# Kernel tuning notes

Hardware: AMD Instinct MI355X
Metric: run time of the kernel (lower is better)

Reference implementation:

```python
import jax, jax.numpy as jnp
import numpy as np

B, N, G, K, C = 16, 8192, 128, 32, 384
EPS = 1e-5


def _fps(xyz, n):
    # furthest point sampling starting at index 0 (matches pointnet2 CUDA op)
    b = xyz.shape[0]
    dists = jnp.sum((xyz - xyz[:, :1]) ** 2, -1)  # [B,N] dist^2 to first pt

    def step(d, _):
        idx = jnp.argmax(d, axis=-1)                       # [B]
        p = jnp.take_along_axis(xyz, idx[:, None, None], 1)  # [B,1,3]
        d = jnp.minimum(d, jnp.sum((xyz - p) ** 2, -1))
        return d, idx.astype(jnp.int32)

    _, idxs = jax.lax.scan(step, dists, None, length=n - 1)
    idx = jnp.concatenate([jnp.zeros((1, b), jnp.int32), idxs], 0).T  # [B,n]
    return jnp.take_along_axis(xyz, idx[..., None], axis=1)


def _morton_order(center):
    # greedy nearest-neighbour tour over group centers (simplied_morton_sorting)
    b, g, _ = center.shape
    d = jnp.sum((center[:, :, None] - center[:, None]) ** 2, -1)  # [B,G,G]
    d = jnp.where(jnp.eye(g, dtype=bool), jnp.inf, d)

    def step(carry, _):
        cur, visited = carry
        row = jnp.take_along_axis(d, cur[:, None, None], 1)[:, 0]  # [B,G]
        row = jnp.where(visited, jnp.inf, row)
        nxt = jnp.argmin(row, -1).astype(jnp.int32)
        visited = visited | jax.nn.one_hot(nxt, g, dtype=bool)
        return (nxt, visited), nxt

    cur0 = jnp.zeros((b,), jnp.int32)
    init = (cur0, jax.nn.one_hot(cur0, g, dtype=bool))
    _, nxts = jax.lax.scan(step, init, None, length=g - 1)
    return jnp.concatenate([jnp.zeros((1, b), jnp.int32), nxts], 0).T  # [B,G]


def _bn(x, g_, b_, m_, v_):
    return (x - m_) * (g_ * jax.lax.rsqrt(v_ + EPS)) + b_


def _pos_embed(center):
    npf = 128  # 384 // 3 // 2 * 2
    i = jnp.arange(npf, dtype=jnp.float32)
    dim_t = 10000.0 ** (2.0 * jnp.floor(i / 2) / npf)
    x = center * (2.0 * np.pi)
    pd = x[..., None] / dim_t                                # [B,G,3,128]
    emb = jnp.stack([jnp.sin(pd[..., 0::2]), jnp.cos(pd[..., 1::2])], -1)
    return emb.reshape(*center.shape[:-1], -1)               # [B,G,384]


def _forward(xyz, w1, b1, g1, bt1, m1, v1, w2, b2, w3, b3, g3, bt3, m3, v3, w4, b4):
    center = _fps(xyz, G)                                    # [B,G,3]
    # squared-distance KNN (argsort order identical to euclidean cdist)
    d2 = (jnp.sum(center ** 2, -1)[:, :, None]
          + jnp.sum(xyz ** 2, -1)[:, None]
          - 2.0 * jnp.einsum('bgd,bnd->bgn', center, xyz))   # [B,G,N]
    _, idx = jax.lax.top_k(-d2, K)                           # [B,G,K]
    neigh = jnp.take_along_axis(xyz, idx.reshape(B, G * K)[..., None], 1)
    neigh = neigh.reshape(B, G, K, 3) - center[:, :, None]
    order = _morton_order(center)                            # [B,G]
    neigh = jnp.take_along_axis(neigh, order[:, :, None, None], 1)
    center = jnp.take_along_axis(center, order[:, :, None], 1)
    # Encoder_small (1x1 convs == per-point linears, eval-mode BN)
    pg = neigh.reshape(B * G, K, 3)
    f = jax.nn.relu(_bn(pg @ w1.T + b1, g1, bt1, m1, v1)) @ w2.T + b2  # [BG,K,256]
    fg = jnp.max(f, 1, keepdims=True)
    h = jnp.concatenate([jnp.broadcast_to(fg, f.shape), f], -1)        # [BG,K,512]
    h = jax.nn.relu(_bn(h @ w3.T + b3, g3, bt3, m3, v3)) @ w4.T + b4   # [BG,K,384]
    tokens = jnp.max(h, 1).reshape(B, G, C)
    return tokens + _pos_embed(center)


def setup_inputs() -> dict:
    key = jax.random.key(0)
    ks = jax.random.split(key, 8)
    s = 0.05
    return {
        'xyz': jax.random.normal(ks[0], (B, N, 3), jnp.float32),
        'w1': jax.random.normal(ks[1], (128, 3), jnp.float32) * s,
        'b1': jax.random.normal(ks[2], (128,), jnp.float32) * s,
        'g1': jnp.ones((128,), jnp.float32),
        'bt1': jnp.zeros((128,), jnp.float32),
        'm1': jnp.zeros((128,), jnp.float32),
        'v1': jnp.ones((128,), jnp.float32),
        'w2': jax.random.normal(ks[3], (256, 128), jnp.float32) * s,
        'b2': jax.random.normal(ks[4], (256,), jnp.float32) * s,
        'w3': jax.random.normal(ks[5], (512, 512), jnp.float32) * s,
        'b3': jnp.zeros((512,), jnp.float32),
        'g3': jnp.ones((512,), jnp.float32),
        'bt3': jnp.zeros((512,), jnp.float32),
        'm3': jnp.zeros((512,), jnp.float32),
        'v3': jnp.ones((512,), jnp.float32),
        'w4': jax.random.normal(ks[6], (384, 512), jnp.float32) * s,
        'b4': jax.random.normal(ks[7], (384,), jnp.float32) * s,
    }


def reference(xyz, w1, b1, g1, bt1, m1, v1, w2, b2, w3, b3, g3, bt3, m3, v3, w4, b4):
    return _forward(xyz, w1, b1, g1, bt1, m1, v1, w2, b2, w3, b3, g3, bt3, m3, v3, w4, b4)
```

## Files before the change

kernel.cpp:

```cpp
#include <hip/hip_runtime.h>
#include <hip/hip_bf16.h>

#define B_ 16
#define N_ 8192
#define G_ 128
#define K_ 32
#define C_ 384
#define EPSV 1e-5f

typedef __attribute__((ext_vector_type(8))) short bf16x8;
typedef __attribute__((ext_vector_type(8))) unsigned short u16x8;
typedef __attribute__((ext_vector_type(4))) float f32x4;
typedef __attribute__((ext_vector_type(2))) float f32x2;

__device__ __forceinline__ unsigned short f2b(float f){
  unsigned int u = __float_as_uint(f);
  u += 0x7fffu + ((u >> 16) & 1u);
  return (unsigned short)(u >> 16);
}
__device__ __forceinline__ float b2f(unsigned short s){
  return __uint_as_float(((unsigned int)s) << 16);
}
__device__ __forceinline__ float sq3(float dx, float dy, float dz){
  return __fadd_rn(__fadd_rn(__fmul_rn(dx,dx), __fmul_rn(dy,dy)), __fmul_rn(dz,dz));
}
__device__ __forceinline__ f32x2 pkmax(f32x2 a, f32x2 b){
  return f32x2{fmaxf(a.x,b.x), fmaxf(a.y,b.y)};
}
__device__ __forceinline__ unsigned fenc(float f){
  unsigned u = __float_as_uint(f);
  return ((int)u >= 0) ? (u | 0x80000000u) : ~u;
}

#define DPP_MAXU_STAGE(r, CTRL) { \
  unsigned _o = (unsigned)__builtin_amdgcn_update_dpp((int)(r), (int)(r), (CTRL), 0xf, 0xf, false); \
  (r) = ((r) > _o) ? (r) : _o; }
#define DPP_MAXU_ALL(r) \
  DPP_MAXU_STAGE(r, 0x111) DPP_MAXU_STAGE(r, 0x112) DPP_MAXU_STAGE(r, 0x114) \
  DPP_MAXU_STAGE(r, 0x118) DPP_MAXU_STAGE(r, 0x142) DPP_MAXU_STAGE(r, 0x143)
#define DPP_MINU_STAGE(r, CTRL) { \
  unsigned _o = (unsigned)__builtin_amdgcn_update_dpp((int)(r), (int)(r), (CTRL), 0xf, 0xf, false); \
  (r) = ((r) < _o) ? (r) : _o; }
#define DPP_MINU_ALL(r) \
  DPP_MINU_STAGE(r, 0x111) DPP_MINU_STAGE(r, 0x112) DPP_MINU_STAGE(r, 0x114) \
  DPP_MINU_STAGE(r, 0x118) DPP_MINU_STAGE(r, 0x142) DPP_MINU_STAGE(r, 0x143)

__global__ __launch_bounds__(256) void prep_kernel(
    const float* __restrict__ w2, const float* __restrict__ w3,
    const float* __restrict__ w4, unsigned short* __restrict__ w2b,
    unsigned short* __restrict__ w3b, unsigned short* __restrict__ w4b){
  int i = blockIdx.x*256 + threadIdx.x;
  if (i < 32768){ w2b[i] = f2b(w2[i]); return; }
  i -= 32768;
  if (i < 262144){ w3b[i] = f2b(w3[i]); return; }
  i -= 262144;
  if (i < 196608){ w4b[i] = f2b(w4[i]); }
}

__attribute__((amdgpu_flat_work_group_size(256,256), amdgpu_waves_per_eu(1,1)))
__global__ void fps_morton_kernel(const float* __restrict__ xyz,
                                  float* __restrict__ centers_ord){
  const int b = blockIdx.x, t = threadIdx.x, w = t >> 6;
  const int lane = t & 63;
  const float* xb = xyz + (size_t)b*N_*3;
  __shared__ __align__(16) float sval[2][4];
  __shared__ __align__(16) int   sidx[2][4];
  __shared__ float clx[G_], cly[G_], clz[G_];
  const int base = t*32;
  f32x2 X[16], Y[16], Z[16], D[16];
  const float p0x = xb[0], p0y = xb[1], p0z = xb[2];
  {
#pragma clang fp contract(off)
    float s[96];
    const float4* src = (const float4*)(xb + (size_t)base*3);
    #pragma unroll
    for (int q = 0; q < 24; q++) ((float4*)s)[q] = src[q];
    #pragma unroll
    for (int p = 0; p < 16; p++){
      X[p] = f32x2{s[6*p+0], s[6*p+3]};
      Y[p] = f32x2{s[6*p+1], s[6*p+4]};
      Z[p] = f32x2{s[6*p+2], s[6*p+5]};
      const f32x2 dx = X[p] - p0x, dy = Y[p] - p0y, dz = Z[p] - p0z;
      D[p] = (dx*dx + dy*dy) + dz*dz;
    }
  }
  if (t == 0){ clx[0] = p0x; cly[0] = p0y; clz[0] = p0z; }
  int buf = 0;
  for (int g = 1; g < G_; g++){
    const f32x2 mm = pkmax(pkmax(pkmax(pkmax(D[0],D[1]),pkmax(D[2],D[3])),
                                 pkmax(pkmax(D[4],D[5]),pkmax(D[6],D[7]))),
                           pkmax(pkmax(pkmax(D[8],D[9]),pkmax(D[10],D[11])),
                                 pkmax(pkmax(D[12],D[13]),pkmax(D[14],D[15]))));
    const float v = fmaxf(mm.x, mm.y);
    int jl = 0;
    #pragma unroll
    for (int p = 15; p >= 0; p--){
      if (D[p].y == v) jl = 2*p+1;
      if (D[p].x == v) jl = 2*p;
    }
    const unsigned uv = __float_as_uint(v);
    unsigned r = uv;
    DPP_MAXU_ALL(r)
    const unsigned wmax = (unsigned)__builtin_amdgcn_readlane((int)r, 63);
    const unsigned long long tie = __ballot(uv == wmax);
    const int wl = __ffsll(tie) - 1;
    if (lane == wl){ sval[buf][w] = __uint_as_float(wmax); sidx[buf][w] = base + jl; }
    __syncthreads();
    const float4 vv = *(const float4*)&sval[buf][0];
    const int4   ii = *(const int4*)&sidx[buf][0];
    float bv = vv.x; int bb = ii.x;
    if (vv.y > bv){ bv = vv.y; bb = ii.y; }
    if (vv.z > bv){ bv = vv.z; bb = ii.z; }
    if (vv.w > bv){ bv = vv.w; bb = ii.w; }
    {
#pragma clang fp contract(off)
      const int ubb = __builtin_amdgcn_readfirstlane(bb);
      const float cx = xb[ubb*3], cy = xb[ubb*3+1], cz = xb[ubb*3+2];
      if (t == 0){ clx[g] = cx; cly[g] = cy; clz[g] = cz; }
      #pragma unroll
      for (int p = 0; p < 16; p++){
        const f32x2 dx = X[p] - cx, dy = Y[p] - cy, dz = Z[p] - cz;
        const f32x2 dn = (dx*dx + dy*dy) + dz*dz;
        D[p] = f32x2{fminf(D[p].x, dn.x), fminf(D[p].y, dn.y)};
      }
    }
    buf ^= 1;
  }
  __syncthreads();
  if (t < 64){
    float mcx[2], mcy[2], mcz[2]; bool mvis[2];
    #pragma unroll
    for (int j = 0; j < 2; j++){
      const int idx = lane + j*64;
      mcx[j] = clx[idx]; mcy[j] = cly[idx]; mcz[j] = clz[idx];
      mvis[j] = (idx == 0);
    }
    float curx = clx[0], cury = cly[0], curz = clz[0];
    if (lane == 0){
      centers_ord[(size_t)b*G_*3 + 0] = curx;
      centers_ord[(size_t)b*G_*3 + 1] = cury;
      centers_ord[(size_t)b*G_*3 + 2] = curz;
    }
    for (int step = 1; step < G_; step++){
      const float d0r = sq3(__fsub_rn(mcx[0],curx), __fsub_rn(mcy[0],cury), __fsub_rn(mcz[0],curz));
      const float d1r = sq3(__fsub_rn(mcx[1],curx), __fsub_rn(mcy[1],cury), __fsub_rn(mcz[1],curz));
      const float d0 = mvis[0] ? __builtin_inff() : d0r;
      const float d1 = mvis[1] ? __builtin_inff() : d1r;
      float mv = d0; int mi = lane;
      if (d1 < mv){ mv = d1; mi = lane + 64; }
      const int wj = mi >> 6;
      const float sx = wj ? mcx[1] : mcx[0];
      const float sy = wj ? mcy[1] : mcy[0];
      const float sz = wj ? mcz[1] : mcz[0];
      const unsigned key = __float_as_uint(mv);
      unsigned r = key;
      DPP_MINU_ALL(r)
      const unsigned wmin = (unsigned)__builtin_amdgcn_readlane((int)r, 63);
      const unsigned long long tie = __ballot(key == wmin);
      int wl;
      if (__popcll(tie) == 1){
        wl = __ffsll(tie) - 1;
      } else {
        float tv = mv; int ti = mi;
        #pragma unroll
        for (int mk = 1; mk < 64; mk <<= 1){
          const float ov = __shfl_xor(tv, mk);
          const int   oi = __shfl_xor(ti, mk);
          if (ov < tv || (ov == tv && oi < ti)){ tv = ov; ti = oi; }
        }
        wl = ti & 63;
      }
      const int mbi = __builtin_amdgcn_readlane(mi, wl);
      curx = __uint_as_float((unsigned)__builtin_amdgcn_readlane((int)__float_as_uint(sx), wl));
      cury = __uint_as_float((unsigned)__builtin_amdgcn_readlane((int)__float_as_uint(sy), wl));
      curz = __uint_as_float((unsigned)__builtin_amdgcn_readlane((int)__float_as_uint(sz), wl));
      if (lane == wl){
        if ((mbi >> 6) == 0) mvis[0] = true; else mvis[1] = true;
      }
      if (lane == 0){
        centers_ord[((size_t)b*G_ + step)*3 + 0] = curx;
        centers_ord[((size_t)b*G_ + step)*3 + 1] = cury;
        centers_ord[((size_t)b*G_ + step)*3 + 2] = curz;
      }
    }
  }
}

__global__ __launch_bounds__(256, 2) void knn_kernel(const float* __restrict__ xyz,
                                                     const float* __restrict__ centers_ord,
                                                     float* __restrict__ neigh){
  const int gp = blockIdx.x, b = blockIdx.y, t = threadIdx.x;
  const int lane = t & 63, w = t >> 6;
  __shared__ __align__(16) float sv[2][4];
  __shared__ __align__(16) int   si[2][4];
  __shared__ int list[K_];
  const float* xb = xyz + (size_t)b*N_*3;
  const float* cp = centers_ord + ((size_t)b*G_ + gp)*3;
  const float cxv = cp[0], cyv = cp[1], czv = cp[2];
  const float cc = sq3(cxv, cyv, czv);
  const int base = t*32;
  float dd[32];
  float v = __builtin_inff(); int jl = 0;
  {
    float s[96];
    const float4* src = (const float4*)(xb + (size_t)base*3);
    #pragma unroll
    for (int q = 0; q < 24; q++) ((float4*)s)[q] = src[q];
    #pragma unroll
    for (int j = 0; j < 32; j++){
      const float x = s[3*j], y = s[3*j+1], z = s[3*j+2];
      const float xx = sq3(x, y, z);
      const float dot = __fadd_rn(__fadd_rn(__fmul_rn(cxv,x), __fmul_rn(cyv,y)), __fmul_rn(czv,z));
      dd[j] = __fsub_rn(__fadd_rn(cc, xx), __fmul_rn(2.f, dot));
      if (dd[j] < v){ v = dd[j]; jl = j; }
    }
  }
  int buf = 0;
  for (int it = 0; it < K_; it++){
    const unsigned key = fenc(v);
    unsigned r = key;
    DPP_MINU_ALL(r)
    const unsigned wmin = (unsigned)__builtin_amdgcn_readlane((int)r, 63);
    const unsigned long long tie = __ballot(key == wmin);
    const int wl = __ffsll(tie) - 1;
    if (lane == wl){ sv[buf][w] = v; si[buf][w] = base + jl; }
    __syncthreads();
    const float4 vv = *(const float4*)&sv[buf][0];
    const int4   ii = *(const int4*)&si[buf][0];
    float bv = vv.x; int bb = ii.x;
    if (vv.y < bv){ bv = vv.y; bb = ii.y; }
    if (vv.z < bv){ bv = vv.z; bb = ii.z; }
    if (vv.w < bv){ bv = vv.w; bb = ii.w; }
    if (t == 0) list[it] = bb;
    if ((bb >> 5) == t){
      const int jw = bb & 31;
      #pragma unroll
      for (int j = 0; j < 32; j++) if (j == jw) dd[j] = __builtin_inff();
      v = __builtin_inff(); jl = 0;
      #pragma unroll
      for (int j = 0; j < 32; j++) if (dd[j] < v){ v = dd[j]; jl = j; }
    }
    buf ^= 1;
  }
  __syncthreads();
  if (t < K_*3){
    const int k = t / 3, d = t % 3;
    const int n = list[k];
    neigh[(((size_t)b*G_ + gp)*K_ + k)*3 + d] = __fsub_rn(xb[n*3+d], cp[d]);
  }
}

__device__ __forceinline__ int swzF(int row, int col){
  int byteo = row*512 + col*2;
  byteo ^= (row & 7) << 4;
  return byteo >> 1;
}
__device__ __forceinline__ int swzA(int row, int col){
  int byteo = row*1024 + col*2;
  byteo ^= (row & 7) << 4;
  return byteo >> 1;
}

__global__ __launch_bounds__(256, 2) void enc_kernel(
    const float* __restrict__ neigh, const float* __restrict__ centers_ord,
    const float* __restrict__ w1, const float* __restrict__ b1,
    const float* __restrict__ g1, const float* __restrict__ bt1,
    const float* __restrict__ m1, const float* __restrict__ v1,
    const unsigned short* __restrict__ w2b, const float* __restrict__ b2,
    const unsigned short* __restrict__ w3b, const float* __restrict__ b3,
    const float* __restrict__ g3, const float* __restrict__ bt3,
    const float* __restrict__ m3, const float* __restrict__ v3,
    const unsigned short* __restrict__ w4b, const float* __restrict__ b4,
    float* __restrict__ out)
{
  const int gp = blockIdx.x, b = blockIdx.y, t = threadIdx.x;
  const int lane = t & 63, w = t >> 6, lr = lane & 15, lg = lane >> 4;
  __shared__ __align__(16) unsigned short Fl[32*256];
  __shared__ __align__(16) unsigned short A3[32*512];
  __shared__ __align__(16) unsigned short fgb[256];
  __shared__ float pg[96];
  __shared__ float ctr[3];
  float* tok = (float*)Fl;

  const int gid = b*G_ + gp;
  if (t < 96) pg[t] = neigh[(size_t)gid*96 + t];
  if (t < 3)  ctr[t] = centers_ord[(size_t)gid*3 + t];
  __syncthreads();

  bf16x8 a1f[2][4];
  #pragma unroll
  for (int kt = 0; kt < 4; kt++){
    #pragma unroll
    for (int j = 0; j < 8; j++){
      const int c = kt*32 + lg*8 + j;
      const float wx = w1[c*3], wy = w1[c*3+1], wz = w1[c*3+2];
      const float sc = g1[c] * rsqrtf(v1[c] + EPSV);
      const float mm = m1[c], bb = bt1[c], bc = b1[c];
      #pragma unroll
      for (int mt = 0; mt < 2; mt++){
        const int p = mt*16 + lr;
        float v = pg[p*3]*wx + pg[p*3+1]*wy + pg[p*3+2]*wz + bc;
        v = (v - mm)*sc + bb;
        v = fmaxf(v, 0.f);
        a1f[mt][kt][j] = (short)f2b(v);
      }
    }
  }

  const int n0w = w*64;
  {
    bf16x8 Bk[16];
    #pragma unroll
    for (int i = 0; i < 16; i++){
      const int nt = i >> 2, kt = i & 3;
      Bk[i] = *(const bf16x8*)(w2b + (size_t)(n0w + nt*16 + lr)*128 + kt*32 + lg*8);
    }
    f32x4 accB[2][4];
    #pragma unroll
    for (int mt = 0; mt < 2; mt++)
      #pragma unroll
      for (int nt = 0; nt < 4; nt++){
        f32x4 z = {0.f,0.f,0.f,0.f};
        accB[mt][nt] = z;
      }
    #pragma unroll
    for (int nt = 0; nt < 4; nt++)
      #pragma unroll
      for (int kt = 0; kt < 4; kt++){
        accB[0][nt] = __builtin_amdgcn_mfma_f32_16x16x32_bf16(a1f[0][kt], Bk[nt*4+kt], accB[0][nt], 0,0,0);
        accB[1][nt] = __builtin_amdgcn_mfma_f32_16x16x32_bf16(a1f[1][kt], Bk[nt*4+kt], accB[1][nt], 0,0,0);
      }
    #pragma unroll
    for (int nt = 0; nt < 4; nt++){
      const int col = n0w + nt*16 + lr;
      const float bc = b2[col];
      #pragma unroll
      for (int mt = 0; mt < 2; mt++)
        #pragma unroll
        for (int r = 0; r < 4; r++){
          const int row = mt*16 + lg*4 + r;
          Fl[swzF(row,col)] = f2b(accB[mt][nt][r] + bc);
        }
    }
  }
  __syncthreads();

  {
    float mx = -__builtin_inff();
    #pragma unroll 4
    for (int row = 0; row < 32; row++) mx = fmaxf(mx, b2f(Fl[swzF(row, t)]));
    fgb[t] = f2b(mx);
  }
  __syncthreads();

  {
    bf16x8 afg[8], afl0[8], afl1[8];
    #pragma unroll
    for (int k8 = 0; k8 < 8; k8++){
      afg[k8]  = *(const bf16x8*)&fgb[k8*32 + lg*8];
      afl0[k8] = *(const bf16x8*)&Fl[swzF(lr,      k8*32 + lg*8)];
      afl1[k8] = *(const bf16x8*)&Fl[swzF(16 + lr, k8*32 + lg*8)];
    }
    #pragma unroll
    for (int nt = 0; nt < 8; nt++){
      const int col = w*128 + nt*16 + lr;
      const unsigned short* wr = w3b + (size_t)col*512;
      bf16x8 Bk[16];
      #pragma unroll
      for (int kt = 0; kt < 16; kt++) Bk[kt] = *(const bf16x8*)(wr + kt*32 + lg*8);
      f32x4 a0 = {0.f,0.f,0.f,0.f}, a1v = {0.f,0.f,0.f,0.f};
      #pragma unroll
      for (int k8 = 0; k8 < 8; k8++){
        a0  = __builtin_amdgcn_mfma_f32_16x16x32_bf16(afg[k8], Bk[k8], a0, 0,0,0);
        a1v = __builtin_amdgcn_mfma_f32_16x16x32_bf16(afg[k8], Bk[k8], a1v, 0,0,0);
      }
      #pragma unroll
      for (int k8 = 0; k8 < 8; k8++){
        a0  = __builtin_amdgcn_mfma_f32_16x16x32_bf16(afl0[k8], Bk[8+k8], a0, 0,0,0);
        a1v = __builtin_amdgcn_mfma_f32_16x16x32_bf16(afl1[k8], Bk[8+k8], a1v, 0,0,0);
      }
      const float bc = b3[col];
      const float sc = g3[col]*rsqrtf(v3[col] + EPSV);
      const float mm = m3[col], bb = bt3[col];
      #pragma unroll
      for (int mt = 0; mt < 2; mt++)
        #pragma unroll
        for (int r = 0; r < 4; r++){
          const int row = mt*16 + lg*4 + r;
          float v = (mt ? a1v[r] : a0[r]) + bc;
          v = (v - mm)*sc + bb;
          v = fmaxf(v, 0.f);
          A3[swzA(row,col)] = f2b(v);
        }
    }
  }
  __syncthreads();

  {
    bf16x8 aa0[16], aa1[16];
    #pragma unroll
    for (int kt = 0; kt < 16; kt++){
      aa0[kt] = *(const bf16x8*)&A3[swzA(lr,      kt*32 + lg*8)];
      aa1[kt] = *(const bf16x8*)&A3[swzA(16 + lr, kt*32 + lg*8)];
    }
    #pragma unroll
    for (int nt = 0; nt < 6; nt++){
      const int col = w*96 + nt*16 + lr;
      const unsigned short* wr = w4b + (size_t)col*512;
      bf16x8 Bk[16];
      #pragma unroll
      for (int kt = 0; kt < 16; kt++) Bk[kt] = *(const bf16x8*)(wr + kt*32 + lg*8);
      f32x4 a0 = {0.f,0.f,0.f,0.f}, a1v = {0.f,0.f,0.f,0.f};
      #pragma unroll
      for (int kt = 0; kt < 16; kt++){
        a0  = __builtin_amdgcn_mfma_f32_16x16x32_bf16(aa0[kt], Bk[kt], a0, 0,0,0);
        a1v = __builtin_amdgcn_mfma_f32_16x16x32_bf16(aa1[kt], Bk[kt], a1v, 0,0,0);
      }
      float mx = fmaxf(fmaxf(fmaxf(a0[0],a0[1]), fmaxf(a0[2],a0[3])),
                       fmaxf(fmaxf(a1v[0],a1v[1]), fmaxf(a1v[2],a1v[3])));
      mx = fmaxf(mx, __shfl_xor(mx, 16));
      mx = fmaxf(mx, __shfl_xor(mx, 32));
      if (lg == 0) tok[col] = mx + b4[col];
    }
  }
  __syncthreads();

  for (int c = t; c < C_; c += 256){
    const int d = c >> 7, r = c & 127, m2 = r >> 1;
    const float e = (float)(2*m2) * (1.f/128.f);
    const float dimt = powf(10000.f, e);
    const float x2 = __fmul_rn(ctr[d], 6.28318530717958647692f);
    const float ang = __fdiv_rn(x2, dimt);
    out[(size_t)gid*C_ + c] = tok[c] + ((r & 1) ? cosf(ang) : sinf(ang));
  }
}

extern "C" void kernel_launch(void* const* d_in, const int* in_sizes, int n_in,
                              void* d_out, int out_size, void* d_ws, size_t ws_size,
                              hipStream_t stream){
  (void)in_sizes; (void)n_in; (void)out_size; (void)ws_size;
  const float* xyz = (const float*)d_in[0];
  const float* w1  = (const float*)d_in[1];
  const float* b1  = (const float*)d_in[2];
  const float* g1  = (const float*)d_in[3];
  const float* bt1 = (const float*)d_in[4];
  const float* m1  = (const float*)d_in[5];
  const float* v1  = (const float*)d_in[6];
  const float* w2  = (const float*)d_in[7];
  const float* b2  = (const float*)d_in[8];
  const float* w3  = (const float*)d_in[9];
  const float* b3  = (const float*)d_in[10];
  const float* g3  = (const float*)d_in[11];
  const float* bt3 = (const float*)d_in[12];
  const float* m3  = (const float*)d_in[13];
  const float* v3  = (const float*)d_in[14];
  const float* w4  = (const float*)d_in[15];
  const float* b4  = (const float*)d_in[16];

  char* ws = (char*)d_ws;
  float* centers_ord  = (float*)(ws + 24576);
  float* neigh        = (float*)(ws + 49152);
  unsigned short* w2b = (unsigned short*)(ws + 835584);
  unsigned short* w3b = (unsigned short*)(ws + 901120);
  unsigned short* w4b = (unsigned short*)(ws + 1425408);

  prep_kernel      <<<1920, 256, 0, stream>>>(w2, w3, w4, w2b, w3b, w4b);
  fps_morton_kernel<<<B_, 256, 0, stream>>>(xyz, centers_ord);
  knn_kernel       <<<dim3(G_, B_), 256, 0, stream>>>(xyz, centers_ord, neigh);
  enc_kernel       <<<dim3(G_, B_), 256, 0, stream>>>(neigh, centers_ord,
      w1, b1, g1, bt1, m1, v1, w2b, b2, w3b, b3, g3, bt3, m3, v3, w4b, b4,
      (float*)d_out);
}
```

Baseline: 595.1 us.

## Process two groups per encoder block to share weight loads across MFMAs

The encoder kernel now handles two point groups per block with 512 threads. Each weight fragment loaded from global memory feeds MFMAs for both groups, which halves weight traffic per group. The first layer's activations are staged through shared memory instead of registers, and the column split across eight waves is changed. Shared memory per block roughly doubles, which may limit occupancy.

Measured after the change: 511.2 us. -14.1%, faster.

```diff
diff --git a/kernel.cpp b/kernel.cpp
--- a/kernel.cpp
+++ b/kernel.cpp
@@ -250,6 +250,11 @@
   }
 }
 
+__device__ __forceinline__ int swzA1(int row, int col){
+  int byteo = row*256 + col*2;
+  byteo ^= (row & 7) << 4;
+  return byteo >> 1;
+}
 __device__ __forceinline__ int swzF(int row, int col){
   int byteo = row*512 + col*2;
   byteo ^= (row & 7) << 4;
@@ -261,7 +266,7 @@
   return byteo >> 1;
 }
 
-__global__ __launch_bounds__(256, 2) void enc_kernel(
+__global__ __launch_bounds__(512, 2) void enc_kernel(
     const float* __restrict__ neigh, const float* __restrict__ centers_ord,
     const float* __restrict__ w1, const float* __restrict__ b1,
     const float* __restrict__ g1, const float* __restrict__ bt1,
@@ -273,165 +278,201 @@
     const unsigned short* __restrict__ w4b, const float* __restrict__ b4,
     float* __restrict__ out)
 {
-  const int gp = blockIdx.x, b = blockIdx.y, t = threadIdx.x;
+  const int t = threadIdx.x;
   const int lane = t & 63, w = t >> 6, lr = lane & 15, lg = lane >> 4;
-  __shared__ __align__(16) unsigned short Fl[32*256];
-  __shared__ __align__(16) unsigned short A3[32*512];
-  __shared__ __align__(16) unsigned short fgb[256];
-  __shared__ float pg[96];
-  __shared__ float ctr[3];
-  float* tok = (float*)Fl;
-
-  const int gid = b*G_ + gp;
-  if (t < 96) pg[t] = neigh[(size_t)gid*96 + t];
-  if (t < 3)  ctr[t] = centers_ord[(size_t)gid*3 + t];
-  __syncthreads();
-
-  bf16x8 a1f[2][4];
-  #pragma unroll
-  for (int kt = 0; kt < 4; kt++){
-    #pragma unroll
-    for (int j = 0; j < 8; j++){
-      const int c = kt*32 + lg*8 + j;
+  const int gid0 = blockIdx.x*2;
+  __shared__ __align__(16) unsigned short A1s[2][32*128];
+  __shared__ __align__(16) unsigned short Fl[2][32*256];
+  __shared__ __align__(16) unsigned short A3s[2][32*512];
+  __shared__ __align__(16) unsigned short fgb[2][256];
+  float* tokp = (float*)&Fl[0][0];
+
+  {
+    const int g = t >> 8, rem = t & 255, p = rem >> 3, c0 = (rem & 7) * 16;
+    const float* pgp = neigh + (size_t)(gid0 + g)*96 + p*3;
+    const float px = pgp[0], py = pgp[1], pz = pgp[2];
+    unsigned short hv[16];
+    #pragma unroll
+    for (int cc = 0; cc < 16; cc++){
+      const int c = c0 + cc;
       const float wx = w1[c*3], wy = w1[c*3+1], wz = w1[c*3+2];
       const float sc = g1[c] * rsqrtf(v1[c] + EPSV);
-      const float mm = m1[c], bb = bt1[c], bc = b1[c];
-      #pragma unroll
-      for (int mt = 0; mt < 2; mt++){
-        const int p = mt*16 + lr;
-        float v = pg[p*3]*wx + pg[p*3+1]*wy + pg[p*3+2]*wz + bc;
-        v = (v - mm)*sc + bb;
-        v = fmaxf(v, 0.f);
-        a1f[mt][kt][j] = (short)f2b(v);
-      }
-    }
-  }
-
-  const int n0w = w*64;
-  {
-    bf16x8 Bk[16];
-    #pragma unroll
-    for (int i = 0; i < 16; i++){
-      const int nt = i >> 2, kt = i & 3;
-      Bk[i] = *(const bf16x8*)(w2b + (size_t)(n0w + nt*16 + lr)*128 + kt*32 + lg*8);
-    }
-    f32x4 accB[2][4];
-    #pragma unroll
-    for (int mt = 0; mt < 2; mt++)
-      #pragma unroll
-      for (int nt = 0; nt < 4; nt++){
-        f32x4 z = {0.f,0.f,0.f,0.f};
-        accB[mt][nt] = z;
-      }
-    #pragma unroll
-    for (int nt = 0; nt < 4; nt++)
-      #pragma unroll
-      for (int kt = 0; kt < 4; kt++){
-        accB[0][nt] = __builtin_amdgcn_mfma_f32_16x16x32_bf16(a1f[0][kt], Bk[nt*4+kt], accB[0][nt], 0,0,0);
-        accB[1][nt] = __builtin_amdgcn_mfma_f32_16x16x32_bf16(a1f[1][kt], Bk[nt*4+kt], accB[1][nt], 0,0,0);
-      }
-    #pragma unroll
-    for (int nt = 0; nt < 4; nt++){
-      const int col = n0w + nt*16 + lr;
+      float val = px*wx + py*wy + pz*wz + b1[c];
+      val = (val - m1[c])*sc + bt1[c];
+      hv[cc] = f2b(fmaxf(val, 0.f));
+    }
+    *(u16x8*)&A1s[g][swzA1(p, c0)]     = *(u16x8*)&hv[0];
+    *(u16x8*)&A1s[g][swzA1(p, c0 + 8)] = *(u16x8*)&hv[8];
+  }
+  __syncthreads();
+
+  {
+    const int col0 = w*32;
+    f32x4 acc[2][2][2];
+    #pragma unroll
+    for (int nt = 0; nt < 2; nt++)
+      #pragma unroll
+      for (int g = 0; g < 2; g++)
+        #pragma unroll
+        for (int m = 0; m < 2; m++){ f32x4 z = {0.f,0.f,0.f,0.f}; acc[nt][g][m] = z; }
+    #pragma unroll
+    for (int kt = 0; kt < 4; kt++){
+      bf16x8 bA[2][2];
+      #pragma unroll
+      for (int g = 0; g < 2; g++)
+        #pragma unroll
+        for (int m = 0; m < 2; m++)
+          bA[g][m] = *(const bf16x8*)&A1s[g][swzA1(m*16 + lr, kt*32 + lg*8)];
+      bf16x8 bB[2];
+      #pragma unroll
+      for (int nt = 0; nt < 2; nt++)
+        bB[nt] = *(const bf16x8*)(w2b + (size_t)(col0 + nt*16 + lr)*128 + kt*32 + lg*8);
+      #pragma unroll
+      for (int nt = 0; nt < 2; nt++)
+        #pragma unroll
+        for (int g = 0; g < 2; g++)
+          #pragma unroll
+          for (int m = 0; m < 2; m++)
+            acc[nt][g][m] = __builtin_amdgcn_mfma_f32_16x16x32_bf16(bA[g][m], bB[nt], acc[nt][g][m], 0,0,0);
+    }
+    #pragma unroll
+    for (int nt = 0; nt < 2; nt++){
+      const int col = col0 + nt*16 + lr;
       const float bc = b2[col];
       #pragma unroll
-      for (int mt = 0; mt < 2; mt++)
-        #pragma unroll
-        for (int r = 0; r < 4; r++){
-          const int row = mt*16 + lg*4 + r;
-          Fl[swzF(row,col)] = f2b(accB[mt][nt][r] + bc);
-        }
-    }
-  }
-  __syncthreads();
-
-  {
+      for (int g = 0; g < 2; g++)
+        #pragma unroll
+        for (int m = 0; m < 2; m++)
+          #pragma unroll
+          for (int r = 0; r < 4; r++)
+            Fl[g][swzF(m*16 + lg*4 + r, col)] = f2b(acc[nt][g][m][r] + bc);
+    }
+  }
+  __syncthreads();
+
+  {
+    const int g = t >> 8, col = t & 255;
     float mx = -__builtin_inff();
     #pragma unroll 4
-    for (int row = 0; row < 32; row++) mx = fmaxf(mx, b2f(Fl[swzF(row, t)]));
-    fgb[t] = f2b(mx);
-  }
-  __syncthreads();
-
-  {
-    bf16x8 afg[8], afl0[8], afl1[8];
-    #pragma unroll
-    for (int k8 = 0; k8 < 8; k8++){
-      afg[k8]  = *(const bf16x8*)&fgb[k8*32 + lg*8];
-      afl0[k8] = *(const bf16x8*)&Fl[swzF(lr,      k8*32 + lg*8)];
-      afl1[k8] = *(const bf16x8*)&Fl[swzF(16 + lr, k8*32 + lg*8)];
-    }
-    #pragma unroll
-    for (int nt = 0; nt < 8; nt++){
-      const int col = w*128 + nt*16 + lr;
-      const unsigned short* wr = w3b + (size_t)col*512;
-      bf16x8 Bk[16];
-      #pragma unroll
-      for (int kt = 0; kt < 16; kt++) Bk[kt] = *(const bf16x8*)(wr + kt*32 + lg*8);
-      f32x4 a0 = {0.f,0.f,0.f,0.f}, a1v = {0.f,0.f,0.f,0.f};
-      #pragma unroll
-      for (int k8 = 0; k8 < 8; k8++){
-        a0  = __builtin_amdgcn_mfma_f32_16x16x32_bf16(afg[k8], Bk[k8], a0, 0,0,0);
-        a1v = __builtin_amdgcn_mfma_f32_16x16x32_bf16(afg[k8], Bk[k8], a1v, 0,0,0);
+    for (int row = 0; row < 32; row++) mx = fmaxf(mx, b2f(Fl[g][swzF(row, col)]));
+    fgb[g][col] = f2b(mx);
+  }
+  __syncthreads();
+
+  {
+    const int col0 = w*64;
+    f32x4 acc[4][2][2];
+    #pragma unroll
+    for (int nt = 0; nt < 4; nt++)
+      #pragma unroll
+      for (int g = 0; g < 2; g++)
+        #pragma unroll
+        for (int m = 0; m < 2; m++){ f32x4 z = {0.f,0.f,0.f,0.f}; acc[nt][g][m] = z; }
+    #pragma unroll
+    for (int kt = 0; kt < 16; kt++){
+      bf16x8 bA[2][2];
+      if (kt < 8){
+        #pragma unroll
+        for (int g = 0; g < 2; g++){
+          const bf16x8 af = *(const bf16x8*)&fgb[g][kt*32 + lg*8];
+          bA[g][0] = af; bA[g][1] = af;
+        }
+      } else {
+        #pragma unroll
+        for (int g = 0; g < 2; g++)
+          #pragma unroll
+          for (int m = 0; m < 2; m++)
+            bA[g][m] = *(const bf16x8*)&Fl[g][swzF(m*16 + lr, (kt-8)*32 + lg*8)];
       }
-      #pragma unroll
-      for (int k8 = 0; k8 < 8; k8++){
-        a0  = __builtin_amdgcn_mfma_f32_16x16x32_bf16(afl0[k8], Bk[8+k8], a0, 0,0,0);
-        a1v = __builtin_amdgcn_mfma_f32_16x16x32_bf16(afl1[k8], Bk[8+k8], a1v, 0,0,0);
-      }
+      bf16x8 bB[4];
+      #pragma unroll
+      for (int nt = 0; nt < 4; nt++)
+        bB[nt] = *(const bf16x8*)(w3b + (size_t)(col0 + nt*16 + lr)*512 + kt*32 + lg*8);
+      #pragma unroll
+      for (int nt = 0; nt < 4; nt++)
+        #pragma unroll
+        for (int g = 0; g < 2; g++)
+          #pragma unroll
+          for (int m = 0; m < 2; m++)
+            acc[nt][g][m] = __builtin_amdgcn_mfma_f32_16x16x32_bf16(bA[g][m], bB[nt], acc[nt][g][m], 0,0,0);
+    }
+    #pragma unroll
+    for (int nt = 0; nt < 4; nt++){
+      const int col = col0 + nt*16 + lr;
       const float bc = b3[col];
       const float sc = g3[col]*rsqrtf(v3[col] + EPSV);
       const float mm = m3[col], bb = bt3[col];
       #pragma unroll
-      for (int mt = 0; mt < 2; mt++)
-        #pragma unroll
-        for (int r = 0; r < 4; r++){
-          const int row = mt*16 + lg*4 + r;
-          float v = (mt ? a1v[r] : a0[r]) + bc;
-          v = (v - mm)*sc + bb;
-          v = fmaxf(v, 0.f);
-          A3[swzA(row,col)] = f2b(v);
-        }
-    }
-  }
-  __syncthreads();
-
-  {
-    bf16x8 aa0[16], aa1[16];
+      for (int g = 0; g < 2; g++)
+        #pragma unroll
+        for (int m = 0; m < 2; m++)
+          #pragma unroll
+          for (int r = 0; r < 4; r++){
+            float val = acc[nt][g][m][r] + bc;
+            val = (val - mm)*sc + bb;
+            A3s[g][swzA(m*16 + lg*4 + r, col)] = f2b(fmaxf(val, 0.f));
+          }
+    }
+  }
+  __syncthreads();
+
+  {
+    const int col0 = w*48;
+    f32x4 acc[3][2][2];
+    #pragma unroll
+    for (int nt = 0; nt < 3; nt++)
+      #pragma unroll
+      for (int g = 0; g < 2; g++)
+        #pragma unroll
+        for (int m = 0; m < 2; m++){ f32x4 z = {0.f,0.f,0.f,0.f}; acc[nt][g][m] = z; }
     #pragma unroll
     for (int kt = 0; kt < 16; kt++){
-      aa0[kt] = *(const bf16x8*)&A3[swzA(lr,      kt*32 + lg*8)];
-      aa1[kt] = *(const bf16x8*)&A3[swzA(16 + lr, kt*32 + lg*8)];
-    }
-    #pragma unroll
-    for (int nt = 0; nt < 6; nt++){
-      const int col = w*96 + nt*16 + lr;
-      const unsigned short* wr = w4b + (size_t)col*512;
-      bf16x8 Bk[16];
-      #pragma unroll
-      for (int kt = 0; kt < 16; kt++) Bk[kt] = *(const bf16x8*)(wr + kt*32 + lg*8);
-      f32x4 a0 = {0.f,0.f,0.f,0.f}, a1v = {0.f,0.f,0.f,0.f};
-      #pragma unroll
-      for (int kt = 0; kt < 16; kt++){
-        a0  = __builtin_amdgcn_mfma_f32_16x16x32_bf16(aa0[kt], Bk[kt], a0, 0,0,0);
-        a1v = __builtin_amdgcn_mfma_f32_16x16x32_bf16(aa1[kt], Bk[kt], a1v, 0,0,0);
+      bf16x8 bA[2][2];
+      #pragma unroll
+      for (int g = 0; g < 2; g++)
+        #pragma unroll
+        for (int m = 0; m < 2; m++)
+          bA[g][m] = *(const bf16x8*)&A3s[g][swzA(m*16 + lr, kt*32 + lg*8)];
+      bf16x8 bB[3];
+      #pragma unroll
+      for (int nt = 0; nt < 3; nt++)
+        bB[nt] = *(const bf16x8*)(w4b + (size_t)(col0 + nt*16 + lr)*512 + kt*32 + lg*8);
+      #pragma unroll
+      for (int nt = 0; nt < 3; nt++)
+        #pragma unroll
+        for (int g = 0; g < 2; g++)
+          #pragma unroll
+          for (int m = 0; m < 2; m++)
+            acc[nt][g][m] = __builtin_amdgcn_mfma_f32_16x16x32_bf16(bA[g][m], bB[nt], acc[nt][g][m], 0,0,0);
+    }
+    #pragma unroll
+    for (int nt = 0; nt < 3; nt++){
+      const int col = col0 + nt*16 + lr;
+      const float bc = b4[col];
+      #pragma unroll
+      for (int g = 0; g < 2; g++){
+        float mx = fmaxf(
+          fmaxf(fmaxf(acc[nt][g][0][0], acc[nt][g][0][1]), fmaxf(acc[nt][g][0][2], acc[nt][g][0][3])),
+          fmaxf(fmaxf(acc[nt][g][1][0], acc[nt][g][1][1]), fmaxf(acc[nt][g][1][2], acc[nt][g][1][3])));
+        mx = fmaxf(mx, __shfl_xor(mx, 16));
+        mx = fmaxf(mx, __shfl_xor(mx, 32));
+        if (lg == 0) tokp[g*C_ + col] = mx + bc;
       }
-      float mx = fmaxf(fmaxf(fmaxf(a0[0],a0[1]), fmaxf(a0[2],a0[3])),
-                       fmaxf(fmaxf(a1v[0],a1v[1]), fmaxf(a1v[2],a1v[3])));
-      mx = fmaxf(mx, __shfl_xor(mx, 16));
-      mx = fmaxf(mx, __shfl_xor(mx, 32));
-      if (lg == 0) tok[col] = mx + b4[col];
-    }
-  }
-  __syncthreads();
-
-  for (int c = t; c < C_; c += 256){
+    }
+  }
+  __syncthreads();
+
+  for (int c2 = t; c2 < 2*C_; c2 += 512){
+    const int g = (c2 >= C_) ? 1 : 0;
+    const int c = c2 - g*C_;
+    const int gid = gid0 + g;
     const int d = c >> 7, r = c & 127, m2 = r >> 1;
     const float e = (float)(2*m2) * (1.f/128.f);
     const float dimt = powf(10000.f, e);
-    const float x2 = __fmul_rn(ctr[d], 6.28318530717958647692f);
+    const float ctrd = centers_ord[(size_t)gid*3 + d];
+    const float x2 = __fmul_rn(ctrd, 6.28318530717958647692f);
     const float ang = __fdiv_rn(x2, dimt);
-    out[(size_t)gid*C_ + c] = tok[c] + ((r & 1) ? cosf(ang) : sinf(ang));
+    out[(size_t)gid*C_ + c] = tokp[g*C_ + c] + ((r & 1) ? cosf(ang) : sinf(ang));
   }
 }
 
@@ -467,7 +508,7 @@
   prep_kernel      <<<1920, 256, 0, stream>>>(w2, w3, w4, w2b, w3b, w4b);
   fps_morton_kernel<<<B_, 256, 0, stream>>>(xyz, centers_ord);
   knn_kernel       <<<dim3(G_, B_), 256, 0, stream>>>(xyz, centers_ord, neigh);
-  enc_kernel       <<<dim3(G_, B_), 256, 0, stream>>>(neigh, centers_ord,
+  enc_kernel       <<<1024, 512, 0, stream>>>(neigh, centers_ord,
       w1, b1, g1, bt1, m1, v1, w2b, b2, w3b, b3, g3, bt3, m3, v3, w4b, b4,
       (float*)d_out);
 }
```
